# Kernel optimization log

Hardware: AMD Instinct MI355X
Metric: run time of the kernel (lower is better)

Reference implementation:

```python
import jax, jax.numpy as jnp
import numpy as np

B, N, E = 16, 512, 6144          # graphs, sites/graph, edges/graph
D = 256                          # embed_dimension
RBF_DIM = 128
M = 6                            # num_messages
MAXZ = 84                        # max_atomic_num
INIT_MAX_DIST, INIT_GAP = 7.0, 30.0


def setup_inputs() -> dict:
    key = jax.random.key(0)
    ks = jax.random.split(key, 20)
    s = 0.02
    inp = {
        "site_class": jax.random.randint(ks[0], (B, N), 0, MAXZ, dtype=jnp.int64),
        "distance": jax.random.uniform(ks[1], (B, E), dtype=jnp.float32) * INIT_MAX_DIST,
        "connectivity": jax.random.randint(ks[2], (B, E, 2), 0, N, dtype=jnp.int64),
        # learned parameters
        "atom_emb": jax.random.normal(ks[3], (MAXZ, D), jnp.float32) * s,
        "mean_emb": jnp.zeros((MAXZ, 1), jnp.float32),  # Constant(output_bias=0.0)
        "centers": jnp.arange(RBF_DIM, dtype=jnp.float32) * (INIT_MAX_DIST / RBF_DIM),
        "gap": jnp.float32(INIT_GAP),
        "bond_W": jax.random.normal(ks[4], (RBF_DIM, D), jnp.float32) * s,
        "bond_b": jnp.zeros((D,), jnp.float32),
        "offset_W": jax.random.normal(ks[5], (D, 1), jnp.float32) * 1e-6,
        "offset_b": jnp.zeros((1,), jnp.float32),
        # per-message EdgeUpdate ConcatDense: Dense(2D, relu) -> Dense(D), input 3D
        "edge_W1": jax.random.normal(ks[6], (M, 3 * D, 2 * D), jnp.float32) * s,
        "edge_b1": jnp.zeros((M, 2 * D), jnp.float32),
        "edge_W2": jax.random.normal(ks[7], (M, 2 * D, D), jnp.float32) * s,
        "edge_b2": jnp.zeros((M, D), jnp.float32),
        # per-message NodeUpdate ConcatDense: input 2D
        "node_W1": jax.random.normal(ks[8], (M, 2 * D, 2 * D), jnp.float32) * s,
        "node_b1": jnp.zeros((M, 2 * D), jnp.float32),
        "node_W2": jax.random.normal(ks[9], (M, 2 * D, D), jnp.float32) * s,
        "node_b2": jnp.zeros((M, D), jnp.float32),
    }
    return inp


def _gather(x, idx):
    # x: [B, N, D], idx: [B, E] -> [B, E, D]
    return x[jnp.arange(x.shape[0])[:, None], idx]


def reference(site_class, distance, connectivity,
              atom_emb, mean_emb, centers, gap, bond_W, bond_b,
              offset_W, offset_b,
              edge_W1, edge_b1, edge_W2, edge_b2,
              node_W1, node_b1, node_W2, node_b2):
    atom_mask = site_class != 0                     # [B, N] (Embedding mask_zero)
    bond_mask = distance != 0.0                     # [B, E] (RBFExpansion mask)

    atom_state = atom_emb[site_class]               # [B, N, D]
    atom_mean = mean_emb[site_class]                # [B, N, 1]

    # RBF expansion: exp(-gap * (d - centers)^2), masked distances -> 1.0
    d = distance[..., None]
    d = jnp.where(d != 0.0, d, 1.0)
    rbf = jnp.exp(-((d - centers) ** 2) * gap)      # [B, E, RBF_DIM]
    bond_state = rbf @ bond_W + bond_b              # [B, E, D]

    bidx = jnp.arange(site_class.shape[0])[:, None]
    idx0 = connectivity[..., 0]                     # scatter target
    idx1 = connectivity[..., 1]                     # message source

    n_msg = edge_W1.shape[0]
    for i in range(n_msg):
        # EdgeUpdate: concat(bond, src_atom, tgt_atom) -> Dense(2D, relu) -> Dense(D)
        src = _gather(atom_state, idx1)
        tgt = _gather(atom_state, idx0)
        h = jnp.concatenate([bond_state, src, tgt], axis=-1)      # [B, E, 3D]
        h = jax.nn.relu(h @ edge_W1[i] + edge_b1[i])
        h = h @ edge_W2[i] + edge_b2[i]
        h = jnp.where(bond_mask[..., None], h, 0.0)
        bond_state = bond_state + h

        # NodeUpdate: concat(src_atom, bond) -> MLP -> segment-sum onto idx0
        src = _gather(atom_state, idx1)
        m = jnp.concatenate([src, bond_state], axis=-1)           # [B, E, 2D]
        m = jax.nn.relu(m @ node_W1[i] + node_b1[i])
        m = m @ node_W2[i] + node_b2[i]
        new_atom = jnp.zeros_like(atom_state).at[bidx, idx0].add(m)
        new_atom = jnp.where(atom_mask[..., None], new_atom, 0.0)
        atom_state = atom_state + new_atom

    atom_mean = atom_mean + (atom_state @ offset_W + offset_b)   # [B, N, 1]

    # masked global average pooling over sites
    mask_f = atom_mask[..., None].astype(atom_mean.dtype)
    pooled = jnp.sum(atom_mean * mask_f, axis=1) / jnp.sum(mask_f, axis=1)
    return pooled  # [B, 1]
```

## Files before the change

### kernel.cpp

```cpp
#include <hip/hip_runtime.h>
#include <hip/hip_bf16.h>
#include <stdint.h>
#include <stddef.h>

#define Bb 16
#define Nn 512
#define Ee 6144
#define Dd 256
#define ROWS (Bb * Ee)
#define HALF (ROWS / 2)

typedef short bf16x8 __attribute__((ext_vector_type(8)));
typedef float f32x4 __attribute__((ext_vector_type(4)));

__device__ __forceinline__ unsigned short f2bf(float f) {
  union { float f; unsigned u; } v; v.f = f;
  return (unsigned short)((v.u + 0x7fffu + ((v.u >> 16) & 1u)) >> 16);
}

__device__ __forceinline__ void gload16(const void* g, void* l) {
  __builtin_amdgcn_global_load_lds(
      (const __attribute__((address_space(1))) void*)g,
      (__attribute__((address_space(3))) void*)l, 16, 0, 0);
}

__global__ void transpose_w(const float* __restrict__ in, unsigned short* __restrict__ out,
                            int K, int Ncol) {
  __shared__ float tile[32][33];
  const float* inb = in + (size_t)blockIdx.z * K * Ncol;
  unsigned short* outb = out + (size_t)blockIdx.z * K * Ncol;
  int bk = blockIdx.x * 32, bn = blockIdx.y * 32;
  int tx = threadIdx.x, ty = threadIdx.y;
#pragma unroll
  for (int i = 0; i < 32; i += 8)
    tile[ty + i][tx] = inb[(size_t)(bk + ty + i) * Ncol + (bn + tx)];
  __syncthreads();
#pragma unroll
  for (int i = 0; i < 32; i += 8)
    outb[(size_t)(bn + ty + i) * K + (bk + tx)] = f2bf(tile[tx][ty + i]);
}

__global__ void atom_init(const int* __restrict__ cls, const float* __restrict__ emb,
                          float* __restrict__ atom, unsigned short* __restrict__ atomBf) {
  int s_ = blockIdx.x, d = threadIdx.x;
  size_t o = (size_t)s_ * Dd + d;
  float v = emb[(size_t)cls[s_] * Dd + d];
  atom[o] = v;
  atomBf[o] = f2bf(v);
}

__global__ void atom_fix(const int* __restrict__ cls, const float* __restrict__ emb,
                         float* __restrict__ atom, unsigned short* __restrict__ atomBf) {
  int s_ = blockIdx.x, d = threadIdx.x;
  size_t o = (size_t)s_ * Dd + d;
  float v = (cls[s_] == 0) ? emb[d] : atom[o];
  atom[o] = v;
  atomBf[o] = f2bf(v);
}

__global__ __launch_bounds__(256, 2) void gemm_rbf(
    const unsigned short* __restrict__ Wt, const float* __restrict__ bias,
    const float* __restrict__ dist, const float* __restrict__ centers,
    const float* __restrict__ gapP, float* __restrict__ bond,
    unsigned short* __restrict__ bondBf) {
  __shared__ __align__(16) unsigned short lA[128 * 64];
  __shared__ __align__(16) unsigned short lB[128 * 64];
  const int t = threadIdx.x;
  const int bm = blockIdx.x * 128, bn = blockIdx.y * 128;
  const int srow = t & 127, skc = (t >> 7) * 32;
  const int m = bm + srow;
  float dval = dist[m]; if (dval == 0.f) dval = 1.f;
  float gapv = *gapP;
  const unsigned short* pBt = Wt + (size_t)(bn + srow) * 128 + skc;
  const int wid = t >> 6, lane = t & 63;
  const int wm = (wid & 1) * 64, wn = (wid >> 1) * 64;
  const int fr = lane & 15, fk0 = (lane >> 4) * 8;
  f32x4 acc[4][4] = {};
  for (int k0 = 0; k0 < 128; k0 += 64) {
    union __align__(16) { unsigned short us[32]; bf16x8 v[4]; } ab, bb;
#pragma unroll
    for (int j = 0; j < 32; j++) {
      float x = dval - centers[k0 + skc + j];
      ab.us[j] = f2bf(__expf(-gapv * x * x));
    }
    const bf16x8* s = (const bf16x8*)(pBt + k0);
#pragma unroll
    for (int c = 0; c < 4; c++) bb.v[c] = s[c];
    __syncthreads();
#pragma unroll
    for (int c = 0; c < 4; c++) {
      int byteo = (skc + c * 8) * 2;
      int swz = byteo ^ ((srow & 7) << 4);
      *(bf16x8*)((char*)lA + srow * 128 + swz) = ab.v[c];
      *(bf16x8*)((char*)lB + srow * 128 + swz) = bb.v[c];
    }
    __syncthreads();
#pragma unroll
    for (int kk = 0; kk < 64; kk += 32) {
      bf16x8 af[4], bfq[4];
#pragma unroll
      for (int f = 0; f < 4; f++) {
        int r = wm + f * 16 + fr;
        af[f] = *(const bf16x8*)((const char*)lA + r * 128 + (((kk + fk0) * 2) ^ ((r & 7) << 4)));
        int cq = wn + f * 16 + fr;
        bfq[f] = *(const bf16x8*)((const char*)lB + cq * 128 + (((kk + fk0) * 2) ^ ((cq & 7) << 4)));
      }
#pragma unroll
      for (int i = 0; i < 4; i++)
#pragma unroll
        for (int j = 0; j < 4; j++)
          acc[i][j] = __builtin_amdgcn_mfma_f32_16x16x32_bf16(af[i], bfq[j], acc[i][j], 0, 0, 0);
    }
  }
#pragma unroll
  for (int i = 0; i < 4; i++)
#pragma unroll
    for (int j = 0; j < 4; j++) {
      int gcol = bn + wn + j * 16 + fr;
      float bvv = bias[gcol];
#pragma unroll
      for (int v = 0; v < 4; v++) {
        int grow = bm + wm + i * 16 + (lane >> 4) * 4 + v;
        float val = acc[i][j][v] + bvv;
        size_t o = (size_t)grow * Dd + gcol;
        bond[o] = val;
        bondBf[o] = f2bf(val);
      }
    }
}

struct GP {
  const unsigned short* Wt;
  const float* bias;
  const unsigned short* bondBf;
  const unsigned short* atomBf;
  const unsigned short* h1;
  const int* conn;
  const float* dist;
  float* bond;
  unsigned short* outH1;
  unsigned short* outBondBf;
  float* atomMaster;
  int rowBase;
};

#define A_EDGE1 0
#define A_NODE1 1
#define A_H1    2
#define EP_H1RELU 0
#define EP_EDGE2  1
#define EP_NODE2  2

template <int K, int NC, int BN, int AL, int EP>
__global__ __launch_bounds__(512, 2) void gemm256(GP p) {
  constexpr int WN = BN / 64;
  constexpr int WM = 8 / WN;
  constexpr int MF = 16 / WM;
  constexpr int ABUF = 32768;
  constexpr int BBUF = BN * 128;
  constexpr int BOFF = 2 * ABUF;
  __shared__ __align__(16) char lds[2 * ABUF + 2 * BBUF];

  const int t = threadIdx.x;
  const int w = t >> 6, l = t & 63;
  constexpr int NT = NC / BN;
  const int bn = (blockIdx.x % NT) * BN;
  const int bm = (blockIdx.x / NT) * 256;

  const char* pR0[4]; const char* pR1[4]; const char* pR2[4];
  const char* pW[WN];
#pragma unroll
  for (int i = 0; i < 4; i++) {
    int r = (w * 4 + i) * 8 + (l >> 3);
    int swz = (((l & 7) ^ (r & 7)) << 4);
    if (AL == A_H1) {
      pR0[i] = (const char*)p.h1 + (size_t)(bm + r) * (K * 2) + swz;
      pR1[i] = pR0[i]; pR2[i] = pR0[i];
    } else {
      int gr = p.rowBase + bm + r;
      int b = gr / Ee;
      int i0 = p.conn[2 * gr], i1 = p.conn[2 * gr + 1];
      const char* bondRow = (const char*)p.bondBf + (size_t)gr * 512 + swz;
      const char* srcRow = (const char*)p.atomBf + ((size_t)b * Nn + i1) * 512 + swz;
      const char* tgtRow = (const char*)p.atomBf + ((size_t)b * Nn + i0) * 512 + swz;
      if (AL == A_EDGE1) { pR0[i] = bondRow; pR1[i] = srcRow; pR2[i] = tgtRow; }
      else               { pR0[i] = srcRow;  pR1[i] = bondRow; pR2[i] = bondRow; }
    }
  }
#pragma unroll
  for (int i = 0; i < WN; i++) {
    int r = (w * WN + i) * 8 + (l >> 3);
    int swz = (((l & 7) ^ (r & 7)) << 4);
    pW[i] = (const char*)p.Wt + (size_t)(bn + r) * (K * 2) + swz;
  }

  const int fr = l & 15;
  const int ck0 = l >> 4;
  const int wr = w / WN, wc = w % WN;
  const int wm = wr * (MF * 16);
  const int wn = wc * 64;

  f32x4 acc[MF][4] = {};

  auto stage = [&](int pb, int k0) {
#pragma unroll
    for (int i = 0; i < 4; i++) {
      const char* src;
      if (AL == A_H1)         src = pR0[i] + k0 * 2;
      else if (AL == A_EDGE1) src = (k0 < 256 ? pR0[i] : (k0 < 512 ? pR1[i] : pR2[i])) + (k0 & 255) * 2;
      else                    src = (k0 < 256 ? pR0[i] : pR1[i]) + (k0 & 255) * 2;
      gload16(src, lds + pb * ABUF + (w * 4 + i) * 1024);
    }
#pragma unroll
    for (int i = 0; i < WN; i++)
      gload16(pW[i] + k0 * 2, lds + BOFF + pb * BBUF + (w * WN + i) * 1024);
  };

  auto compute = [&](int pb) {
#pragma unroll
    for (int kk = 0; kk < 2; kk++) {
      const int ck = kk * 4 + ck0;
      bf16x8 av[MF], bv[4];
#pragma unroll
      for (int f = 0; f < MF; f++) {
        int r = wm + f * 16 + fr;
        av[f] = *(const bf16x8*)(lds + pb * ABUF + r * 128 + ((ck ^ (r & 7)) << 4));
      }
#pragma unroll
      for (int n = 0; n < 4; n++) {
        int rq = wn + n * 16 + fr;
        bv[n] = *(const bf16x8*)(lds + BOFF + pb * BBUF + rq * 128 + ((ck ^ (rq & 7)) << 4));
      }
#pragma unroll
      for (int f = 0; f < MF; f++)
#pragma unroll
        for (int n = 0; n < 4; n++)
          acc[f][n] = __builtin_amdgcn_mfma_f32_16x16x32_bf16(av[f], bv[n], acc[f][n], 0, 0, 0);
    }
  };

  constexpr int nT = K / 64;
  stage(0, 0);
  __syncthreads();
  for (int tt = 0; tt < nT; tt++) {
    int pb = tt & 1;
    if (tt + 1 < nT) stage(pb ^ 1, (tt + 1) * 64);
    compute(pb);
    __syncthreads();
  }

  float bias4[4];
#pragma unroll
  for (int n = 0; n < 4; n++) bias4[n] = p.bias[bn + wn + n * 16 + fr];

#pragma unroll
  for (int f = 0; f < MF; f++) {
#pragma unroll
    for (int v = 0; v < 4; v++) {
      int lrow = bm + wm + f * 16 + (l >> 4) * 4 + v;
      if (EP == EP_H1RELU) {
#pragma unroll
        for (int n = 0; n < 4; n++) {
          int gcol = bn + wn + n * 16 + fr;
          float val = acc[f][n][v] + bias4[n];
          p.outH1[(size_t)lrow * 512 + gcol] = f2bf(fmaxf(val, 0.f));
        }
      } else if (EP == EP_EDGE2) {
        int grow = p.rowBase + lrow;
        if (p.dist[grow] != 0.f) {
#pragma unroll
          for (int n = 0; n < 4; n++) {
            int gcol = bn + wn + n * 16 + fr;
            size_t o = (size_t)grow * Dd + gcol;
            float nv = p.bond[o] + acc[f][n][v] + bias4[n];
            p.bond[o] = nv;
            p.outBondBf[o] = f2bf(nv);
          }
        }
      } else {
        int grow = p.rowBase + lrow;
        int b = grow / Ee;
        int tg = p.conn[2 * grow];
        float* dst = p.atomMaster + ((size_t)b * Nn + tg) * Dd;
#pragma unroll
        for (int n = 0; n < 4; n++) {
          int gcol = bn + wn + n * 16 + fr;
          atomicAdd(dst + gcol, acc[f][n][v] + bias4[n]);
        }
      }
    }
  }
}

__global__ void pool_k(const float* __restrict__ atom, const int* __restrict__ cls,
                       const float* __restrict__ meanEmb, const float* __restrict__ oW,
                       const float* __restrict__ ob, float* __restrict__ out) {
  __shared__ float w[Dd];
  __shared__ float red[256];
  __shared__ float redc[256];
  int b = blockIdx.x, t = threadIdx.x;
  w[t] = oW[t];
  __syncthreads();
  float sum = 0.f, cnt = 0.f;
  for (int n = t; n < Nn; n += 256) {
    int site = b * Nn + n;
    int c = cls[site];
    const float* a = atom + (size_t)site * Dd;
    float dot = 0.f;
    for (int d = 0; d < Dd; d++) dot += a[d] * w[d];
    if (c != 0) { sum += meanEmb[c] + dot + ob[0]; cnt += 1.f; }
  }
  red[t] = sum; redc[t] = cnt;
  __syncthreads();
  for (int s = 128; s > 0; s >>= 1) {
    if (t < s) { red[t] += red[t + s]; redc[t] += redc[t + s]; }
    __syncthreads();
  }
  if (t == 0) out[b] = red[0] / redc[0];
}

extern "C" void kernel_launch(void* const* d_in, const int* in_sizes, int n_in,
                              void* d_out, int out_size, void* d_ws, size_t ws_size,
                              hipStream_t stream) {
  const int* site_class = (const int*)d_in[0];
  const float* distance = (const float*)d_in[1];
  const int* conn       = (const int*)d_in[2];
  const float* atom_emb = (const float*)d_in[3];
  const float* mean_emb = (const float*)d_in[4];
  const float* centers  = (const float*)d_in[5];
  const float* gapP     = (const float*)d_in[6];
  const float* bond_W   = (const float*)d_in[7];
  const float* bond_b   = (const float*)d_in[8];
  const float* offset_W = (const float*)d_in[9];
  const float* offset_b = (const float*)d_in[10];
  const float* edge_W1  = (const float*)d_in[11];
  const float* edge_b1  = (const float*)d_in[12];
  const float* edge_W2  = (const float*)d_in[13];
  const float* edge_b2  = (const float*)d_in[14];
  const float* node_W1  = (const float*)d_in[15];
  const float* node_b1  = (const float*)d_in[16];
  const float* node_W2  = (const float*)d_in[17];
  const float* node_b2  = (const float*)d_in[18];

  char* ws = (char*)d_ws;
  float* atom            = (float*)(ws + 0);
  unsigned short* atomBf = (unsigned short*)(ws + 8388608);
  float* bond            = (float*)(ws + 12582912);
  unsigned short* bondBf = (unsigned short*)(ws + 113246208);
  unsigned short* h1     = (unsigned short*)(ws + 163577856);
  unsigned short* bWT    = (unsigned short*)(ws + 213909504);
  unsigned short* eW1T   = (unsigned short*)(ws + 213975040);
  unsigned short* eW2T   = (unsigned short*)(ws + 218693632);
  unsigned short* nW1T   = (unsigned short*)(ws + 220266496);
  unsigned short* nW2T   = (unsigned short*)(ws + 223412224);

  dim3 tb(32, 8);
  transpose_w<<<dim3(4, 8, 1), tb, 0, stream>>>(bond_W, bWT, 128, 256);
  transpose_w<<<dim3(24, 16, 6), tb, 0, stream>>>(edge_W1, eW1T, 768, 512);
  transpose_w<<<dim3(16, 8, 6), tb, 0, stream>>>(edge_W2, eW2T, 512, 256);
  transpose_w<<<dim3(16, 16, 6), tb, 0, stream>>>(node_W1, nW1T, 512, 512);
  transpose_w<<<dim3(16, 8, 6), tb, 0, stream>>>(node_W2, nW2T, 512, 256);

  atom_init<<<Bb * Nn, 256, 0, stream>>>(site_class, atom_emb, atom, atomBf);
  gemm_rbf<<<dim3(768, 2), 256, 0, stream>>>(bWT, bond_b, distance, centers, gapP, bond, bondBf);

  GP base{};
  base.conn = conn; base.dist = distance;
  base.bondBf = bondBf; base.atomBf = atomBf; base.h1 = h1;
  base.bond = bond; base.outH1 = h1; base.outBondBf = bondBf; base.atomMaster = atom;

  for (int i = 0; i < 6; i++) {
    for (int h = 0; h < 2; h++) {
      GP q = base; q.rowBase = h * HALF;
      q.Wt = eW1T + (size_t)i * 512 * 768; q.bias = edge_b1 + i * 512;
      gemm256<768, 512, 256, A_EDGE1, EP_H1RELU><<<384, 512, 0, stream>>>(q);
      GP q2 = base; q2.rowBase = h * HALF;
      q2.Wt = eW2T + (size_t)i * 256 * 512; q2.bias = edge_b2 + i * 256;
      gemm256<512, 256, 128, A_H1, EP_EDGE2><<<384, 512, 0, stream>>>(q2);
    }
    for (int h = 0; h < 2; h++) {
      GP q = base; q.rowBase = h * HALF;
      q.Wt = nW1T + (size_t)i * 512 * 512; q.bias = node_b1 + i * 512;
      gemm256<512, 512, 256, A_NODE1, EP_H1RELU><<<384, 512, 0, stream>>>(q);
      GP q2 = base; q2.rowBase = h * HALF;
      q2.Wt = nW2T + (size_t)i * 256 * 512; q2.bias = node_b2 + i * 256;
      gemm256<512, 256, 128, A_H1, EP_NODE2><<<384, 512, 0, stream>>>(q2);
    }
    atom_fix<<<Bb * Nn, 256, 0, stream>>>(site_class, atom_emb, atom, atomBf);
  }

  pool_k<<<Bb, 256, 0, stream>>>(atom, site_class, mean_emb, offset_W, offset_b, (float*)d_out);
}
```

Before: 2.368 ms.

## Fuse two-layer edge and node MLPs into one kernel keeping hidden activations in LDS

Each ConcatDense MLP becomes one kernel. The first layer is computed in two 256-column passes, and its ReLU'd bf16 output is written to a swizzled LDS buffer that feeds the second layer directly. Accumulation happens in registers across both passes. This removes the global write and read of the 512-wide hidden tensor and halves the number of GEMM launches per message. The costs are higher register pressure from holding two accumulator sets, a 160KB LDS footprint that allows only one block per CU, and smaller 128-row tiles.

```diff
diff --git a/kernel.cpp b/kernel.cpp
--- a/kernel.cpp
+++ b/kernel.cpp
@@ -8,7 +8,6 @@
 #define Ee 6144
 #define Dd 256
 #define ROWS (Bb * Ee)
-#define HALF (ROWS / 2)
 
 typedef short bf16x8 __attribute__((ext_vector_type(8)));
 typedef float f32x4 __attribute__((ext_vector_type(4)));
@@ -129,163 +128,196 @@
     }
 }
 
-struct GP {
-  const unsigned short* Wt;
-  const float* bias;
+struct FP {
+  const unsigned short* Wt1;
+  const unsigned short* Wt2;
+  const float* b1;
+  const float* b2;
   const unsigned short* bondBf;
   const unsigned short* atomBf;
-  const unsigned short* h1;
   const int* conn;
   const float* dist;
   float* bond;
-  unsigned short* outH1;
   unsigned short* outBondBf;
   float* atomMaster;
-  int rowBase;
 };
 
-#define A_EDGE1 0
-#define A_NODE1 1
-#define A_H1    2
-#define EP_H1RELU 0
-#define EP_EDGE2  1
-#define EP_NODE2  2
-
-template <int K, int NC, int BN, int AL, int EP>
-__global__ __launch_bounds__(512, 2) void gemm256(GP p) {
-  constexpr int WN = BN / 64;
-  constexpr int WM = 8 / WN;
-  constexpr int MF = 16 / WM;
-  constexpr int ABUF = 32768;
-  constexpr int BBUF = BN * 128;
-  constexpr int BOFF = 2 * ABUF;
-  __shared__ __align__(16) char lds[2 * ABUF + 2 * BBUF];
+#define A_EDGE 0
+#define A_NODE 1
+#define EP_EDGE 0
+#define EP_NODE 1
+
+template <int K1, int AL, int EP>
+__global__ __launch_bounds__(512, 2) void fused_mlp(FP p) {
+  __shared__ __align__(16) char lds[163840];
+  constexpr int AOFF = 0, WOFF = 32768, HOFF = 98304;
+  constexpr int nK1 = K1 / 64;
 
   const int t = threadIdx.x;
   const int w = t >> 6, l = t & 63;
-  constexpr int NT = NC / BN;
-  const int bn = (blockIdx.x % NT) * BN;
-  const int bm = (blockIdx.x / NT) * 256;
-
-  const char* pR0[4]; const char* pR1[4]; const char* pR2[4];
-  const char* pW[WN];
+  const int bm = blockIdx.x * 128;
+
+  const int swz = ((l & 7) ^ (l >> 3)) << 4;
+
+  const char* pA0[2]; const char* pA1[2]; const char* pA2[2];
+#pragma unroll
+  for (int i = 0; i < 2; i++) {
+    int r = (w * 2 + i) * 8 + (l >> 3);
+    int gr = bm + r;
+    int b = gr / Ee;
+    int i0 = p.conn[2 * gr], i1 = p.conn[2 * gr + 1];
+    const char* bondRow = (const char*)p.bondBf + (size_t)gr * 512 + swz;
+    const char* srcRow  = (const char*)p.atomBf + ((size_t)b * Nn + i1) * 512 + swz;
+    const char* tgtRow  = (const char*)p.atomBf + ((size_t)b * Nn + i0) * 512 + swz;
+    if (AL == A_EDGE) { pA0[i] = bondRow; pA1[i] = srcRow; pA2[i] = tgtRow; }
+    else              { pA0[i] = srcRow;  pA1[i] = bondRow; pA2[i] = bondRow; }
+  }
+  const char* pW1[4]; const char* pW2[4];
 #pragma unroll
   for (int i = 0; i < 4; i++) {
-    int r = (w * 4 + i) * 8 + (l >> 3);
-    int swz = (((l & 7) ^ (r & 7)) << 4);
-    if (AL == A_H1) {
-      pR0[i] = (const char*)p.h1 + (size_t)(bm + r) * (K * 2) + swz;
-      pR1[i] = pR0[i]; pR2[i] = pR0[i];
-    } else {
-      int gr = p.rowBase + bm + r;
-      int b = gr / Ee;
-      int i0 = p.conn[2 * gr], i1 = p.conn[2 * gr + 1];
-      const char* bondRow = (const char*)p.bondBf + (size_t)gr * 512 + swz;
-      const char* srcRow = (const char*)p.atomBf + ((size_t)b * Nn + i1) * 512 + swz;
-      const char* tgtRow = (const char*)p.atomBf + ((size_t)b * Nn + i0) * 512 + swz;
-      if (AL == A_EDGE1) { pR0[i] = bondRow; pR1[i] = srcRow; pR2[i] = tgtRow; }
-      else               { pR0[i] = srcRow;  pR1[i] = bondRow; pR2[i] = bondRow; }
-    }
-  }
-#pragma unroll
-  for (int i = 0; i < WN; i++) {
-    int r = (w * WN + i) * 8 + (l >> 3);
-    int swz = (((l & 7) ^ (r & 7)) << 4);
-    pW[i] = (const char*)p.Wt + (size_t)(bn + r) * (K * 2) + swz;
+    int rw = (w * 4 + i) * 8 + (l >> 3);
+    pW1[i] = (const char*)p.Wt1 + (size_t)rw * (K1 * 2) + swz;
+    pW2[i] = (const char*)p.Wt2 + (size_t)rw * 1024 + swz;
   }
 
   const int fr = l & 15;
-  const int ck0 = l >> 4;
-  const int wr = w / WN, wc = w % WN;
-  const int wm = wr * (MF * 16);
-  const int wn = wc * 64;
-
-  f32x4 acc[MF][4] = {};
-
-  auto stage = [&](int pb, int k0) {
-#pragma unroll
-    for (int i = 0; i < 4; i++) {
+  const int q4 = l >> 4;
+  const int wm = (w >> 2) * 64;
+  const int wn = (w & 3) * 64;
+
+  auto stageA = [&](int pb, int k0) {
+#pragma unroll
+    for (int i = 0; i < 2; i++) {
       const char* src;
-      if (AL == A_H1)         src = pR0[i] + k0 * 2;
-      else if (AL == A_EDGE1) src = (k0 < 256 ? pR0[i] : (k0 < 512 ? pR1[i] : pR2[i])) + (k0 & 255) * 2;
-      else                    src = (k0 < 256 ? pR0[i] : pR1[i]) + (k0 & 255) * 2;
-      gload16(src, lds + pb * ABUF + (w * 4 + i) * 1024);
-    }
-#pragma unroll
-    for (int i = 0; i < WN; i++)
-      gload16(pW[i] + k0 * 2, lds + BOFF + pb * BBUF + (w * WN + i) * 1024);
+      if (AL == A_EDGE) {
+        int seg = k0 >> 8;
+        src = (seg == 0 ? pA0[i] : (seg == 1 ? pA1[i] : pA2[i])) + (k0 & 255) * 2;
+      } else {
+        src = (k0 < 256 ? pA0[i] : pA1[i]) + (k0 & 255) * 2;
+      }
+      gload16(src, lds + AOFF + pb * 16384 + (w * 2 + i) * 1024);
+    }
   };
-
-  auto compute = [&](int pb) {
-#pragma unroll
-    for (int kk = 0; kk < 2; kk++) {
-      const int ck = kk * 4 + ck0;
-      bf16x8 av[MF], bv[4];
-#pragma unroll
-      for (int f = 0; f < MF; f++) {
-        int r = wm + f * 16 + fr;
-        av[f] = *(const bf16x8*)(lds + pb * ABUF + r * 128 + ((ck ^ (r & 7)) << 4));
-      }
-#pragma unroll
-      for (int n = 0; n < 4; n++) {
-        int rq = wn + n * 16 + fr;
-        bv[n] = *(const bf16x8*)(lds + BOFF + pb * BBUF + rq * 128 + ((ck ^ (rq & 7)) << 4));
-      }
-#pragma unroll
-      for (int f = 0; f < MF; f++)
-#pragma unroll
-        for (int n = 0; n < 4; n++)
-          acc[f][n] = __builtin_amdgcn_mfma_f32_16x16x32_bf16(av[f], bv[n], acc[f][n], 0, 0, 0);
-    }
+  auto stageW1 = [&](int pb, int pass, int kb) {
+#pragma unroll
+    for (int i = 0; i < 4; i++)
+      gload16(pW1[i] + (size_t)pass * 512 * K1 + kb * 128,
+              lds + WOFF + pb * 32768 + (w * 4 + i) * 1024);
   };
-
-  constexpr int nT = K / 64;
-  stage(0, 0);
-  __syncthreads();
-  for (int tt = 0; tt < nT; tt++) {
-    int pb = tt & 1;
-    if (tt + 1 < nT) stage(pb ^ 1, (tt + 1) * 64);
-    compute(pb);
+  auto stageW2 = [&](int pb, int pass, int kb) {
+#pragma unroll
+    for (int i = 0; i < 4; i++)
+      gload16(pW2[i] + pass * 512 + kb * 128,
+              lds + WOFF + pb * 32768 + (w * 4 + i) * 1024);
+  };
+
+  f32x4 acc2[4][4] = {};
+
+  for (int pass = 0; pass < 2; ++pass) {
+    f32x4 acc1[4][4] = {};
+    stageA(0, 0);
+    stageW1(0, pass, 0);
     __syncthreads();
-  }
-
-  float bias4[4];
-#pragma unroll
-  for (int n = 0; n < 4; n++) bias4[n] = p.bias[bn + wn + n * 16 + fr];
-
-#pragma unroll
-  for (int f = 0; f < MF; f++) {
+    for (int kb = 0; kb < nK1; ++kb) {
+      int pb = kb & 1;
+      if (kb + 1 < nK1) { stageA(pb ^ 1, (kb + 1) * 64); stageW1(pb ^ 1, pass, kb + 1); }
+#pragma unroll
+      for (int kk = 0; kk < 2; kk++) {
+        const int ck = kk * 4 + q4;
+        bf16x8 av[4], bv[4];
+#pragma unroll
+        for (int f = 0; f < 4; f++) {
+          int r = wm + f * 16 + fr;
+          av[f] = *(const bf16x8*)(lds + AOFF + pb * 16384 + r * 128 + ((ck ^ (r & 7)) << 4));
+        }
+#pragma unroll
+        for (int n = 0; n < 4; n++) {
+          int rq = wn + n * 16 + fr;
+          bv[n] = *(const bf16x8*)(lds + WOFF + pb * 32768 + rq * 128 + ((ck ^ (rq & 7)) << 4));
+        }
+#pragma unroll
+        for (int f = 0; f < 4; f++)
+#pragma unroll
+          for (int n = 0; n < 4; n++)
+            acc1[f][n] = __builtin_amdgcn_mfma_f32_16x16x32_bf16(av[f], bv[n], acc1[f][n], 0, 0, 0);
+      }
+      __syncthreads();
+    }
+    stageW2(0, pass, 0);
+    {
+      float b1v[4];
+#pragma unroll
+      for (int n = 0; n < 4; n++) b1v[n] = p.b1[pass * 256 + wn + n * 16 + fr];
+#pragma unroll
+      for (int f = 0; f < 4; f++)
+#pragma unroll
+        for (int n = 0; n < 4; n++) {
+          int col2 = (wn + n * 16 + fr) * 2;
+#pragma unroll
+          for (int v = 0; v < 4; v++) {
+            int row = wm + f * 16 + q4 * 4 + v;
+            float val = fmaxf(acc1[f][n][v] + b1v[n], 0.f);
+            *(unsigned short*)(lds + HOFF + row * 512 + (col2 ^ ((row & 7) << 4))) = f2bf(val);
+          }
+        }
+    }
+    __syncthreads();
+    for (int kb = 0; kb < 4; ++kb) {
+      int pb = kb & 1;
+      if (kb + 1 < 4) stageW2(pb ^ 1, pass, kb + 1);
+#pragma unroll
+      for (int kk = 0; kk < 2; kk++) {
+        const int ck = kk * 4 + q4;
+        const int hc = kb * 8 + ck;
+        bf16x8 av[4], bv[4];
+#pragma unroll
+        for (int f = 0; f < 4; f++) {
+          int r = wm + f * 16 + fr;
+          av[f] = *(const bf16x8*)(lds + HOFF + r * 512 + ((hc << 4) ^ ((r & 7) << 4)));
+        }
+#pragma unroll
+        for (int n = 0; n < 4; n++) {
+          int rq = wn + n * 16 + fr;
+          bv[n] = *(const bf16x8*)(lds + WOFF + pb * 32768 + rq * 128 + ((ck ^ (rq & 7)) << 4));
+        }
+#pragma unroll
+        for (int f = 0; f < 4; f++)
+#pragma unroll
+          for (int n = 0; n < 4; n++)
+            acc2[f][n] = __builtin_amdgcn_mfma_f32_16x16x32_bf16(av[f], bv[n], acc2[f][n], 0, 0, 0);
+      }
+      __syncthreads();
+    }
+  }
+
+  float b2v[4];
+#pragma unroll
+  for (int n = 0; n < 4; n++) b2v[n] = p.b2[wn + n * 16 + fr];
+
+#pragma unroll
+  for (int f = 0; f < 4; f++) {
 #pragma unroll
     for (int v = 0; v < 4; v++) {
-      int lrow = bm + wm + f * 16 + (l >> 4) * 4 + v;
-      if (EP == EP_H1RELU) {
-#pragma unroll
-        for (int n = 0; n < 4; n++) {
-          int gcol = bn + wn + n * 16 + fr;
-          float val = acc[f][n][v] + bias4[n];
-          p.outH1[(size_t)lrow * 512 + gcol] = f2bf(fmaxf(val, 0.f));
-        }
-      } else if (EP == EP_EDGE2) {
-        int grow = p.rowBase + lrow;
+      int grow = bm + wm + f * 16 + q4 * 4 + v;
+      if (EP == EP_EDGE) {
         if (p.dist[grow] != 0.f) {
 #pragma unroll
           for (int n = 0; n < 4; n++) {
-            int gcol = bn + wn + n * 16 + fr;
+            int gcol = wn + n * 16 + fr;
             size_t o = (size_t)grow * Dd + gcol;
-            float nv = p.bond[o] + acc[f][n][v] + bias4[n];
+            float nv = p.bond[o] + acc2[f][n][v] + b2v[n];
             p.bond[o] = nv;
             p.outBondBf[o] = f2bf(nv);
           }
         }
       } else {
-        int grow = p.rowBase + lrow;
         int b = grow / Ee;
         int tg = p.conn[2 * grow];
         float* dst = p.atomMaster + ((size_t)b * Nn + tg) * Dd;
 #pragma unroll
         for (int n = 0; n < 4; n++) {
-          int gcol = bn + wn + n * 16 + fr;
-          atomicAdd(dst + gcol, acc[f][n][v] + bias4[n]);
+          int gcol = wn + n * 16 + fr;
+          atomicAdd(dst + gcol, acc2[f][n][v] + b2v[n]);
         }
       }
     }
@@ -347,12 +379,11 @@
   unsigned short* atomBf = (unsigned short*)(ws + 8388608);
   float* bond            = (float*)(ws + 12582912);
   unsigned short* bondBf = (unsigned short*)(ws + 113246208);
-  unsigned short* h1     = (unsigned short*)(ws + 163577856);
-  unsigned short* bWT    = (unsigned short*)(ws + 213909504);
-  unsigned short* eW1T   = (unsigned short*)(ws + 213975040);
-  unsigned short* eW2T   = (unsigned short*)(ws + 218693632);
-  unsigned short* nW1T   = (unsigned short*)(ws + 220266496);
-  unsigned short* nW2T   = (unsigned short*)(ws + 223412224);
+  unsigned short* bWT    = (unsigned short*)(ws + 163577856);
+  unsigned short* eW1T   = (unsigned short*)(ws + 163643392);
+  unsigned short* eW2T   = (unsigned short*)(ws + 168361984);
+  unsigned short* nW1T   = (unsigned short*)(ws + 169934848);
+  unsigned short* nW2T   = (unsigned short*)(ws + 173080576);
 
   dim3 tb(32, 8);
   transpose_w<<<dim3(4, 8, 1), tb, 0, stream>>>(bond_W, bWT, 128, 256);
@@ -364,28 +395,21 @@
   atom_init<<<Bb * Nn, 256, 0, stream>>>(site_class, atom_emb, atom, atomBf);
   gemm_rbf<<<dim3(768, 2), 256, 0, stream>>>(bWT, bond_b, distance, centers, gapP, bond, bondBf);
 
-  GP base{};
-  base.conn = conn; base.dist = distance;
-  base.bondBf = bondBf; base.atomBf = atomBf; base.h1 = h1;
-  base.bond = bond; base.outH1 = h1; base.outBondBf = bondBf; base.atomMaster = atom;
+  FP base{};
+  base.bondBf = bondBf; base.atomBf = atomBf; base.conn = conn; base.dist = distance;
+  base.bond = bond; base.outBondBf = bondBf; base.atomMaster = atom;
 
   for (int i = 0; i < 6; i++) {
-    for (int h = 0; h < 2; h++) {
-      GP q = base; q.rowBase = h * HALF;
-      q.Wt = eW1T + (size_t)i * 512 * 768; q.bias = edge_b1 + i * 512;
-      gemm256<768, 512, 256, A_EDGE1, EP_H1RELU><<<384, 512, 0, stream>>>(q);
-      GP q2 = base; q2.rowBase = h * HALF;
-      q2.Wt = eW2T + (size_t)i * 256 * 512; q2.bias = edge_b2 + i * 256;
-      gemm256<512, 256, 128, A_H1, EP_EDGE2><<<384, 512, 0, stream>>>(q2);
-    }
-    for (int h = 0; h < 2; h++) {
-      GP q = base; q.rowBase = h * HALF;
-      q.Wt = nW1T + (size_t)i * 512 * 512; q.bias = node_b1 + i * 512;
-      gemm256<512, 512, 256, A_NODE1, EP_H1RELU><<<384, 512, 0, stream>>>(q);
-      GP q2 = base; q2.rowBase = h * HALF;
-      q2.Wt = nW2T + (size_t)i * 256 * 512; q2.bias = node_b2 + i * 256;
-      gemm256<512, 256, 128, A_H1, EP_NODE2><<<384, 512, 0, stream>>>(q2);
-    }
+    FP q = base;
+    q.Wt1 = eW1T + (size_t)i * 512 * 768; q.b1 = edge_b1 + i * 512;
+    q.Wt2 = eW2T + (size_t)i * 256 * 512; q.b2 = edge_b2 + i * 256;
+    fused_mlp<768, A_EDGE, EP_EDGE><<<768, 512, 0, stream>>>(q);
+
+    FP r = base;
+    r.Wt1 = nW1T + (size_t)i * 512 * 512; r.b1 = node_b1 + i * 512;
+    r.Wt2 = nW2T + (size_t)i * 256 * 512; r.b2 = node_b2 + i * 256;
+    fused_mlp<512, A_NODE, EP_NODE><<<768, 512, 0, stream>>>(r);
+
     atom_fix<<<Bb * Nn, 256, 0, stream>>>(site_class, atom_emb, atom, atomBf);
   }
 
```

Result: slower. 2.766 ms (+16.8%).
